# Performance work log

Hardware: AMD Instinct MI355X
Metric: run time of the kernel (lower is better)

Reference implementation:

```python
import jax, jax.numpy as jnp
import numpy as np

B, S, D, H, L, V, DFF = 8, 1024, 256, 8, 4, 100, 1024
EPS = 1e-5


def _pos_encodings(seq_len, d):
    # Faithful to SinusoidalPositionalEmbedding (NOTE: original uses sin for both halves)
    pos = jnp.arange(seq_len, dtype=jnp.float32)[:, None]        # [S,1]
    freqs = jnp.arange(d, dtype=jnp.float32)[None, :]            # [1,D]
    sin_even = jnp.sin(pos / 10000.0 ** (freqs[:, 0::2] / d))    # [S,D/2]
    sin_odd = jnp.sin(pos / 10000.0 ** (freqs[:, 1::2] / d))     # [S,D/2]
    return jnp.concatenate([sin_even, sin_odd], axis=1)          # [S,D]


def _self_attention_mask(sequence_length, seq_len):
    # create_self_attention_mask with causal=True; assumes max(sequence_length)==seq_len
    r = jnp.arange(seq_len)[None, :]                             # [1,S]
    m = (r < sequence_length[:, None]).astype(jnp.float32)       # [B,S]
    m = m[:, :, None] * m[:, None, :]                            # [B,S,S]
    causal = jnp.tril(jnp.ones((seq_len, seq_len), jnp.float32))
    return m * causal                                            # [B,S,S]


def setup_inputs() -> dict:
    key = jax.random.key(0)
    ks = jax.random.split(key, 20)
    n = lambda k, shape, s=0.02: (jax.random.normal(k, shape) * s).astype(jnp.float32)
    return {
        "output_ids": jax.random.randint(ks[0], (B, S), 0, V),
        "target_sequence_length": jnp.full((B,), S, dtype=jnp.int32),
        "embedding": n(ks[1], (V, D), 1.0),
        "Wq": n(ks[2], (L, D, D)), "bq": jnp.zeros((L, D), jnp.float32),
        "Wk": n(ks[3], (L, D, D)), "bk": jnp.zeros((L, D), jnp.float32),
        "Wv": n(ks[4], (L, D, D)), "bv": jnp.zeros((L, D), jnp.float32),
        "Wo": n(ks[5], (L, D, D)), "bo": jnp.zeros((L, D), jnp.float32),
        "W1": n(ks[6], (L, D, DFF)), "b1": jnp.zeros((L, DFF), jnp.float32),
        "W2": n(ks[7], (L, DFF, D)), "b2": jnp.zeros((L, D), jnp.float32),
        "g1": jnp.ones((L, D), jnp.float32), "be1": jnp.zeros((L, D), jnp.float32),
        "g2": jnp.ones((L, D), jnp.float32), "be2": jnp.zeros((L, D), jnp.float32),
        "Wc": n(ks[8], (D, V)), "bc": jnp.zeros((V,), jnp.float32),
    }


def _forward(output_ids, target_sequence_length, embedding, Wq, bq, Wk, bk, Wv, bv,
             Wo, bo, W1, b1, W2, b2, g1, be1, g2, be2, Wc, bc):
    Bn, Sn = output_ids.shape
    d = embedding.shape[1]
    x = embedding[output_ids] + _pos_encodings(Sn, d)[None]      # [B,S,D]
    mask = _self_attention_mask(target_sequence_length, Sn)[:, None] > 0  # [B,1,S,S] bool

    def ln(h, g, b):
        m = h.mean(-1, keepdims=True)
        v = jnp.var(h, axis=-1, keepdims=True)
        return (h - m) / jnp.sqrt(v + EPS) * g + b

    def step(x, p):
        wq, bq_, wk, bk_, wv, bv_, wo, bo_, w1, b1_, w2, b2_, g1_, be1_, g2_, be2_ = p
        q = (x @ wq + bq_).reshape(Bn, Sn, H, -1)
        k = (x @ wk + bk_).reshape(Bn, Sn, H, -1)
        v = (x @ wv + bv_).reshape(Bn, Sn, H, -1)
        dh = q.shape[-1]
        scores = jnp.einsum('bqhd,bkhd->bhqk', q, k) / jnp.sqrt(jnp.float32(dh))
        attn = jax.nn.softmax(jnp.where(mask, scores, -1e9), axis=-1)
        attn = jnp.where(mask, attn, 0.0)                        # post-softmax mask (as original)
        y = jnp.einsum('bhqk,bkhd->bqhd', attn, v).reshape(Bn, Sn, -1)
        y = y @ wo + bo_
        x = ln(x + y, g1_, be1_)
        ff = jax.nn.relu(x @ w1 + b1_) @ w2 + b2_
        x = ln(x + ff, g2_, be2_)
        return x, None

    x, _ = jax.lax.scan(step, x, (Wq, bq, Wk, bk, Wv, bv, Wo, bo, W1, b1, W2, b2, g1, be1, g2, be2))
    return x @ Wc + bc                                           # logits [B,S,V]


def reference(output_ids, target_sequence_length, embedding, Wq, bq, Wk, bk, Wv, bv,
              Wo, bo, W1, b1, W2, b2, g1, be1, g2, be2, Wc, bc):
    return _forward(output_ids, target_sequence_length, embedding, Wq, bq, Wk, bk, Wv, bv,
                    Wo, bo, W1, b1, W2, b2, g1, be1, g2, be2, Wc, bc)
```

## Files before the change

kernel.cpp:

```cpp
#include <hip/hip_runtime.h>
#include <hip/hip_bf16.h>
#include <stdint.h>

#define B_   8
#define S_   1024
#define D_   256
#define H_   8
#define DH_  32
#define L_   4
#define V_   100
#define DFF_ 1024
#define M_   (B_*S_)

using bf16 = __hip_bfloat16;
typedef __bf16 bf16x8 __attribute__((ext_vector_type(8)));
typedef float  f32x4  __attribute__((ext_vector_type(4)));

static __device__ __forceinline__ float b2f(unsigned short u) {
  union { unsigned int i; float f; } w; w.i = ((unsigned int)u) << 16; return w.f;
}

static __device__ __forceinline__ void load_lds16(const void* g, void* l) {
  __builtin_amdgcn_global_load_lds((const __attribute__((address_space(1))) void*)g,
                                   (__attribute__((address_space(3))) void*)l,
                                   16, 0, 0);
}

#define SRC_CHS(tid)  ((((tid) & 3) ^ (((tid) >> 3) & 3)) * 8)
#define FRAG_Q8(quad, l15)  (((quad) ^ (((l15) >> 1) & 3)) * 8)

template<int CTRL>
static __device__ __forceinline__ float dppf(float v) {
  union { float f; int i; } a, r;
  a.f = v;
  r.i = __builtin_amdgcn_update_dpp(0, a.i, CTRL, 0xF, 0xF, true);
  return r.f;
}
static __device__ __forceinline__ float red_sum16(float v) {
  v += dppf<0xB1>(v);
  v += dppf<0x4E>(v);
  v += dppf<0x141>(v);
  v += dppf<0x140>(v);
  return v;
}

__global__ void prep_t(const float* __restrict__ Wq, const float* __restrict__ Wk,
                       const float* __restrict__ Wv, const float* __restrict__ Wo,
                       const float* __restrict__ W1, const float* __restrict__ W2,
                       const float* __restrict__ Wc,
                       const float* __restrict__ bq, const float* __restrict__ bk,
                       const float* __restrict__ bv,
                       bf16* __restrict__ WqkvT, bf16* __restrict__ WoT,
                       bf16* __restrict__ W1T, bf16* __restrict__ W2T,
                       bf16* __restrict__ WcT, float* __restrict__ bqkv)
{
  const int z = blockIdx.z;
  if (z == 25) {
    if (blockIdx.x || blockIdx.y) return;
    const int tid = threadIdx.y*32 + threadIdx.x;
    for (int i = tid; i < L_*768; i += 256) {
      const int l2 = i / 768, j = i % 768;
      const float* src = (j < 256) ? bq : (j < 512) ? bk : bv;
      bqkv[i] = src[l2*256 + (j & 255)];
    }
    return;
  }
  const float* src; bf16* dst; int R, C, Cd;
  if (z < 12) {
    const int l = z / 3, w = z % 3;
    src = ((w == 0) ? Wq : (w == 1) ? Wk : Wv) + (size_t)l*65536;
    R = 256; C = 256; Cd = 256;
    dst = WqkvT + (size_t)l*196608 + (size_t)w*65536;
  } else if (z < 16) {
    const int l = z - 12;
    src = Wo + (size_t)l*65536; R = 256; C = 256; Cd = 256;
    dst = WoT + (size_t)l*65536;
  } else if (z < 20) {
    const int l = z - 16;
    src = W1 + (size_t)l*262144; R = 256; C = 1024; Cd = 1024;
    dst = W1T + (size_t)l*262144;
  } else if (z < 24) {
    const int l = z - 20;
    src = W2 + (size_t)l*262144; R = 1024; C = 256; Cd = 256;
    dst = W2T + (size_t)l*262144;
  } else {
    src = Wc; R = 256; C = 100; Cd = 128;
    dst = WcT;
  }
  const int c0 = blockIdx.x*32, r0 = blockIdx.y*32;
  if (c0 >= Cd || r0 >= R) return;
  __shared__ float t[32][33];
  #pragma unroll
  for (int i = 0; i < 4; ++i) {
    const int r = r0 + threadIdx.y + i*8;
    const int c = c0 + threadIdx.x;
    t[threadIdx.y + i*8][threadIdx.x] = (r < R && c < C) ? src[(size_t)r*C + c] : 0.f;
  }
  __syncthreads();
  #pragma unroll
  for (int i = 0; i < 4; ++i) {
    const int c = c0 + threadIdx.y + i*8;
    const int r = r0 + threadIdx.x;
    if (c < Cd && r < R)
      dst[(size_t)c*R + r] = (bf16)t[threadIdx.x][threadIdx.y + i*8];
  }
}

__global__ void embed_kernel(const int* __restrict__ ids, const float* __restrict__ emb,
                             bf16* __restrict__ x)
{
  const int bs = blockIdx.x;
  const int d  = threadIdx.x;
  const int s  = bs & (S_-1);
  const int id = ids[bs];
  const int f  = (d < 128) ? (2*d) : (2*(d-128)+1);
  const float inv = powf(10000.f, -(float)f * (1.f/256.f));
  const float pe  = sinf((float)s * inv);
  x[(size_t)bs*D_ + d] = (bf16)(emb[(size_t)id*D_ + d] + pe);
}

__global__ __launch_bounds__(256) void gemm_qkv(
    const bf16* __restrict__ A, const bf16* __restrict__ BT,
    const float* __restrict__ bias,
    bf16* __restrict__ qp, bf16* __restrict__ kp, bf16* __restrict__ vt)
{
  __shared__ bf16 As[128*32];
  __shared__ bf16 Bs[64*32];
  __shared__ bf16 Vs[64][136];
  const int tid  = threadIdx.x;
  const int lane = tid & 63, wave = tid >> 6;
  const int quad = lane >> 4, l15 = lane & 15;
  const int m0 = blockIdx.x * 128;
  const int n0 = blockIdx.y * 64;
  const int wm = (wave & 1) * 64;
  const int wn = (wave >> 1) * 32;
  const int K = 256;

  const bf16* a0 = A  + (size_t)m0 * K;
  const bf16* b0 = BT + (size_t)n0 * K;
  const int row = tid >> 2;
  const int chs = SRC_CHS(tid);
  const int q8  = FRAG_Q8(quad, l15);

  f32x4 acc[4][2] = {};

  for (int k0 = 0; k0 < K; k0 += 32) {
    __syncthreads();
    load_lds16(a0 + (size_t)row*K      + k0 + chs, (char*)As + (size_t)wave*1024);
    load_lds16(a0 + (size_t)(row+64)*K + k0 + chs, (char*)As + 4096 + (size_t)wave*1024);
    load_lds16(b0 + (size_t)row*K      + k0 + chs, (char*)Bs + (size_t)wave*1024);
    __syncthreads();
    bf16x8 af[4], bfr[2];
    #pragma unroll
    for (int mt = 0; mt < 4; ++mt)
      af[mt] = *(const bf16x8*)(As + (wm + mt*16 + l15)*32 + q8);
    #pragma unroll
    for (int nt = 0; nt < 2; ++nt)
      bfr[nt] = *(const bf16x8*)(Bs + (wn + nt*16 + l15)*32 + q8);
    #pragma unroll
    for (int mt = 0; mt < 4; ++mt)
      #pragma unroll
      for (int nt = 0; nt < 2; ++nt)
        acc[mt][nt] = __builtin_amdgcn_mfma_f32_16x16x32_bf16(af[mt], bfr[nt], acc[mt][nt], 0, 0, 0);
  }

  const int seg = n0 >> 8;
  const int b  = m0 >> 10;
  const int s0 = m0 & 1023;

  if (seg < 2) {
    bf16* dst = seg ? kp : qp;
    const float sc = seg ? 1.f : 0.17677669529663687f;
    #pragma unroll
    for (int nt = 0; nt < 2; ++nt) {
      const int n  = n0 + wn + nt*16 + l15;
      const int nn = n & 255;
      const int h = nn >> 5, d = nn & 31;
      const float bvs = bias[n];
      bf16* hb = dst + (((size_t)b*H_ + h)*S_)*DH_ + d;
      #pragma unroll
      for (int mt = 0; mt < 4; ++mt) {
        const int ml = wm + mt*16 + quad*4;
        #pragma unroll
        for (int r = 0; r < 4; ++r)
          hb[(size_t)(s0 + ml + r)*DH_] = (bf16)((acc[mt][nt][r] + bvs) * sc);
      }
    }
  } else {
    #pragma unroll
    for (int nt = 0; nt < 2; ++nt) {
      const int nl = wn + nt*16 + l15;
      const float bvs = bias[n0 + nl];
      #pragma unroll
      for (int mt = 0; mt < 4; ++mt) {
        const int ml = wm + mt*16 + quad*4;
        #pragma unroll
        for (int r = 0; r < 4; ++r)
          Vs[nl][ml + r] = (bf16)(acc[mt][nt][r] + bvs);
      }
    }
    __syncthreads();
    #pragma unroll
    for (int t = 0; t < 2; ++t) {
      const int vrow = (tid >> 3) + 32*t;
      const int soff = (tid & 7) * 16;
      const int nn = (n0 + vrow) & 255;
      const int h = nn >> 5, d = nn & 31;
      bf16* dst = vt + (((size_t)b*H_ + h)*DH_ + d)*S_ + s0 + soff;
      *(bf16x8*)dst       = *(const bf16x8*)&Vs[vrow][soff];
      *(bf16x8*)(dst + 8) = *(const bf16x8*)&Vs[vrow][soff + 8];
    }
  }
}

template<bool RELU, bool OUT_BF16>
__global__ __launch_bounds__(256) void gemm_bt(
    const bf16* __restrict__ A, const bf16* __restrict__ BT,
    const float* __restrict__ bias, void* __restrict__ C,
    int M, int N, int K)
{
  __shared__ bf16 As[128*32];
  __shared__ bf16 Bs[64*32];
  const int tid  = threadIdx.x;
  const int lane = tid & 63, wave = tid >> 6;
  const int quad = lane >> 4, l15 = lane & 15;
  const int m0 = blockIdx.x * 128;
  const int n0 = blockIdx.y * 64;
  const int wm = (wave & 1) * 64;
  const int wn = (wave >> 1) * 32;

  const bf16* a0 = A  + (size_t)m0 * K;
  const bf16* b0 = BT + (size_t)n0 * K;
  const int row = tid >> 2;
  const int chs = SRC_CHS(tid);
  const int q8  = FRAG_Q8(quad, l15);

  f32x4 acc[4][2] = {};

  for (int k0 = 0; k0 < K; k0 += 32) {
    __syncthreads();
    load_lds16(a0 + (size_t)row*K      + k0 + chs, (char*)As + (size_t)wave*1024);
    load_lds16(a0 + (size_t)(row+64)*K + k0 + chs, (char*)As + 4096 + (size_t)wave*1024);
    load_lds16(b0 + (size_t)row*K      + k0 + chs, (char*)Bs + (size_t)wave*1024);
    __syncthreads();
    bf16x8 af[4], bfr[2];
    #pragma unroll
    for (int mt = 0; mt < 4; ++mt)
      af[mt] = *(const bf16x8*)(As + (wm + mt*16 + l15)*32 + q8);
    #pragma unroll
    for (int nt = 0; nt < 2; ++nt)
      bfr[nt] = *(const bf16x8*)(Bs + (wn + nt*16 + l15)*32 + q8);
    #pragma unroll
    for (int mt = 0; mt < 4; ++mt)
      #pragma unroll
      for (int nt = 0; nt < 2; ++nt)
        acc[mt][nt] = __builtin_amdgcn_mfma_f32_16x16x32_bf16(af[mt], bfr[nt], acc[mt][nt], 0, 0, 0);
  }

  #pragma unroll
  for (int nt = 0; nt < 2; ++nt) {
    const int n = n0 + wn + nt*16 + l15;
    const float bvs = bias[n];
    #pragma unroll
    for (int mt = 0; mt < 4; ++mt) {
      const int mr = m0 + wm + mt*16 + quad*4;
      #pragma unroll
      for (int r = 0; r < 4; ++r) {
        float v = acc[mt][nt][r] + bvs;
        if (RELU) v = fmaxf(v, 0.f);
        if (OUT_BF16) ((bf16*)C)[(size_t)(mr + r)*N + n] = (bf16)v;
        else          ((float*)C)[(size_t)(mr + r)*N + n] = v;
      }
    }
  }
}

template<bool RELU, bool OUT_BF16, bool NMASK>
__global__ __launch_bounds__(256) void gemm_bt64(
    const bf16* __restrict__ A, const bf16* __restrict__ BT,
    const float* __restrict__ bias, void* __restrict__ C,
    int M, int N, int K)
{
  __shared__ bf16 As[64*32];
  __shared__ bf16 Bs[64*32];
  const int tid  = threadIdx.x;
  const int lane = tid & 63, wave = tid >> 6;
  const int quad = lane >> 4, l15 = lane & 15;
  const int m0 = blockIdx.x * 64;
  const int n0 = blockIdx.y * 64;
  const int wm = (wave & 1) * 32;
  const int wn = (wave >> 1) * 32;

  const bf16* a0 = A  + (size_t)m0 * K;
  const bf16* b0 = BT + (size_t)n0 * K;
  const int row = tid >> 2;
  const int chs = SRC_CHS(tid);
  const int q8  = FRAG_Q8(quad, l15);

  f32x4 acc[2][2] = {};

  for (int k0 = 0; k0 < K; k0 += 32) {
    __syncthreads();
    load_lds16(a0 + (size_t)row*K + k0 + chs, (char*)As + (size_t)wave*1024);
    load_lds16(b0 + (size_t)row*K + k0 + chs, (char*)Bs + (size_t)wave*1024);
    __syncthreads();
    bf16x8 af[2], bfr[2];
    #pragma unroll
    for (int mt = 0; mt < 2; ++mt)
      af[mt] = *(const bf16x8*)(As + (wm + mt*16 + l15)*32 + q8);
    #pragma unroll
    for (int nt = 0; nt < 2; ++nt)
      bfr[nt] = *(const bf16x8*)(Bs + (wn + nt*16 + l15)*32 + q8);
    #pragma unroll
    for (int mt = 0; mt < 2; ++mt)
      #pragma unroll
      for (int nt = 0; nt < 2; ++nt)
        acc[mt][nt] = __builtin_amdgcn_mfma_f32_16x16x32_bf16(af[mt], bfr[nt], acc[mt][nt], 0, 0, 0);
  }

  #pragma unroll
  for (int nt = 0; nt < 2; ++nt) {
    const int n = n0 + wn + nt*16 + l15;
    if (NMASK && n >= N) continue;
    const float bvs = bias[n];
    #pragma unroll
    for (int mt = 0; mt < 2; ++mt) {
      const int mr = m0 + wm + mt*16 + quad*4;
      #pragma unroll
      for (int r = 0; r < 4; ++r) {
        float v = acc[mt][nt][r] + bvs;
        if (RELU) v = fmaxf(v, 0.f);
        if (OUT_BF16) ((bf16*)C)[(size_t)(mr + r)*N + n] = (bf16)v;
        else          ((float*)C)[(size_t)(mr + r)*N + n] = v;
      }
    }
  }
}

__global__ __launch_bounds__(256) void gemm_ln(
    const bf16* __restrict__ A, const bf16* __restrict__ BT,
    const float* __restrict__ bias, const float* __restrict__ g,
    const float* __restrict__ be, bf16* xio, int K)
{
  __shared__ bf16 As[16*32];
  __shared__ bf16 Bs[256*32];
  __shared__ bf16 Xs[16][264];
  __shared__ float sums[4][16][2];

  const int tid  = threadIdx.x;
  const int lane = tid & 63, wave = tid >> 6;
  const int quad = lane >> 4, l15 = lane & 15;
  const int m0 = blockIdx.x * 16;
  const int wn = wave * 64;

  const bf16* a0 = A + (size_t)m0 * K;
  const int chs = SRC_CHS(tid);
  const int q8  = FRAG_Q8(quad, l15);

  f32x4 acc[4] = {};

  for (int k0 = 0; k0 < K; k0 += 32) {
    __syncthreads();
    if (wave == 0)
      load_lds16(a0 + (size_t)(lane >> 2)*K + k0 + SRC_CHS(lane), (char*)As);
    #pragma unroll
    for (int j = 0; j < 4; ++j)
      load_lds16(BT + (size_t)(64*j + (tid >> 2))*K + k0 + chs,
                 (char*)Bs + j*4096 + (size_t)wave*1024);
    __syncthreads();
    const bf16x8 af = *(const bf16x8*)(As + l15*32 + q8);
    #pragma unroll
    for (int nt = 0; nt < 4; ++nt) {
      const bf16x8 bfr = *(const bf16x8*)(Bs + (wn + nt*16 + l15)*32 + q8);
      acc[nt] = __builtin_amdgcn_mfma_f32_16x16x32_bf16(af, bfr, acc[nt], 0, 0, 0);
    }
  }

  {
    const int xr = tid >> 4, xc = (tid & 15) * 16;
    const bf16* src = xio + (size_t)(m0 + xr)*D_ + xc;
    *(bf16x8*)&Xs[xr][xc]     = *(const bf16x8*)src;
    *(bf16x8*)&Xs[xr][xc + 8] = *(const bf16x8*)(src + 8);
  }
  __syncthreads();

  float v[4][4];
  float bvs[4];
  #pragma unroll
  for (int nt = 0; nt < 4; ++nt) bvs[nt] = bias[wn + nt*16 + l15];
  #pragma unroll
  for (int r = 0; r < 4; ++r) {
    const int rr = quad*4 + r;
    float ls = 0.f, lq = 0.f;
    #pragma unroll
    for (int nt = 0; nt < 4; ++nt) {
      const float y = acc[nt][r] + bvs[nt];
      const float xv = b2f(*(const unsigned short*)&Xs[rr][wn + nt*16 + l15]);
      const float vv = xv + y;
      v[r][nt] = vv;
      ls += vv;
      lq += vv*vv;
    }
    ls = red_sum16(ls);
    lq = red_sum16(lq);
    if (l15 == 0) { sums[wave][rr][0] = ls; sums[wave][rr][1] = lq; }
  }
  __syncthreads();

  float gv[4], bev[4];
  #pragma unroll
  for (int nt = 0; nt < 4; ++nt) {
    gv[nt]  = g[wn + nt*16 + l15];
    bev[nt] = be[wn + nt*16 + l15];
  }
  #pragma unroll
  for (int r = 0; r < 4; ++r) {
    const int rr = quad*4 + r;
    const float ts = sums[0][rr][0] + sums[1][rr][0] + sums[2][rr][0] + sums[3][rr][0];
    const float tq = sums[0][rr][1] + sums[1][rr][1] + sums[2][rr][1] + sums[3][rr][1];
    const float mean = ts * (1.f/256.f);
    const float var  = tq * (1.f/256.f) - mean*mean;
    const float inv  = rsqrtf(var + 1e-5f);
    #pragma unroll
    for (int nt = 0; nt < 4; ++nt) {
      const bf16 o = (bf16)((v[r][nt] - mean)*inv*gv[nt] + bev[nt]);
      Xs[rr][wn + nt*16 + l15] = o;
    }
  }
  __syncthreads();

  {
    const int xr = tid >> 4, xc = (tid & 15) * 16;
    bf16* dst = xio + (size_t)(m0 + xr)*D_ + xc;
    *(bf16x8*)dst       = *(const bf16x8*)&Xs[xr][xc];
    *(bf16x8*)(dst + 8) = *(const bf16x8*)&Xs[xr][xc + 8];
  }
}

#define PSTR 68
__global__ __launch_bounds__(256) void attn_kernel(
    const bf16* __restrict__ qp, const bf16* __restrict__ kp,
    const bf16* __restrict__ vt, const int* __restrict__ tsl,
    bf16* __restrict__ out)
{
  const int h = blockIdx.y, b = blockIdx.z;
  const int lane = threadIdx.x & 63, wave = threadIdx.x >> 6;
  const int quad = lane >> 4, l15 = lane & 15;
  const int sid = blockIdx.x + wave*16;
  const int q0 = sid*16;
  const int len = tsl[b];

  __shared__ bf16 Pl[4][16*PSTR];

  const size_t bh = (size_t)b*H_ + h;
  const bf16* qb = qp + bh*S_*DH_;
  const bf16* kb = kp + bh*S_*DH_;
  const bf16* vb = vt + bh*DH_*S_;

  const bf16x8 qf = *(const bf16x8*)(qb + (size_t)(q0 + l15)*DH_ + quad*8);

  float lacc[4] = {0.f, 0.f, 0.f, 0.f};
  f32x4 o0 = {0.f,0.f,0.f,0.f}, o1 = {0.f,0.f,0.f,0.f};

  bf16* pw = &Pl[wave][0];
  const int qrow0 = q0 + quad*4;
  const bool full = (len >= S_);
  const int dt = sid >> 2;

  for (int ks = 0; ks <= dt; ++ks) {
    const int k0 = ks*64;
    f32x4 s[4];
    #pragma unroll
    for (int nt = 0; nt < 4; ++nt) {
      const bf16x8 kf = *(const bf16x8*)(kb + (size_t)(k0 + nt*16 + l15)*DH_ + quad*8);
      const f32x4 z = {0.f,0.f,0.f,0.f};
      s[nt] = __builtin_amdgcn_mfma_f32_16x16x32_bf16(qf, kf, z, 0, 0, 0);
    }
    float p[4][4];
    if (full && ks < dt) {
      #pragma unroll
      for (int nt = 0; nt < 4; ++nt)
        #pragma unroll
        for (int r = 0; r < 4; ++r)
          p[nt][r] = __expf(s[nt][r]);
    } else {
      #pragma unroll
      for (int nt = 0; nt < 4; ++nt) {
        const int kpos = k0 + nt*16 + l15;
        #pragma unroll
        for (int r = 0; r < 4; ++r) {
          const int qr = qrow0 + r;
          const bool ok = (kpos <= qr) && (kpos < len) && (qr < len);
          p[nt][r] = ok ? __expf(s[nt][r]) : 0.f;
        }
      }
    }
    #pragma unroll
    for (int r = 0; r < 4; ++r)
      lacc[r] += (p[0][r] + p[1][r]) + (p[2][r] + p[3][r]);
    #pragma unroll
    for (int nt = 0; nt < 4; ++nt)
      #pragma unroll
      for (int r = 0; r < 4; ++r)
        pw[(quad*4+r)*PSTR + nt*16 + l15] = (bf16)p[nt][r];
    asm volatile("s_waitcnt lgkmcnt(0)" ::: "memory");
    #pragma unroll
    for (int kc = 0; kc < 2; ++kc) {
      const bf16x8 pf = *(const bf16x8*)(pw + l15*PSTR + kc*32 + quad*8);
      const bf16x8 vf0 = *(const bf16x8*)(vb + (size_t)l15*S_ + k0 + kc*32 + quad*8);
      o0 = __builtin_amdgcn_mfma_f32_16x16x32_bf16(pf, vf0, o0, 0, 0, 0);
      const bf16x8 vf1 = *(const bf16x8*)(vb + (size_t)(16 + l15)*S_ + k0 + kc*32 + quad*8);
      o1 = __builtin_amdgcn_mfma_f32_16x16x32_bf16(pf, vf1, o1, 0, 0, 0);
    }
  }

  bf16* ob = out + (size_t)b*S_*D_ + h*DH_;
  #pragma unroll
  for (int r = 0; r < 4; ++r) {
    const float l = red_sum16(lacc[r]);
    const float inv = 1.f / fmaxf(l, 1e-30f);
    const size_t rowoff = (size_t)(q0 + quad*4 + r)*D_;
    ob[rowoff + l15]      = (bf16)(o0[r]*inv);
    ob[rowoff + 16 + l15] = (bf16)(o1[r]*inv);
  }
}

extern "C" void kernel_launch(void* const* d_in, const int* in_sizes, int n_in,
                              void* d_out, int out_size, void* d_ws, size_t ws_size,
                              hipStream_t stream)
{
  const int*   ids = (const int*)d_in[0];
  const int*   tsl = (const int*)d_in[1];
  const float* emb = (const float*)d_in[2];
  const float* Wq  = (const float*)d_in[3];
  const float* bq  = (const float*)d_in[4];
  const float* Wk  = (const float*)d_in[5];
  const float* bk  = (const float*)d_in[6];
  const float* Wv  = (const float*)d_in[7];
  const float* bv  = (const float*)d_in[8];
  const float* Wo  = (const float*)d_in[9];
  const float* bo  = (const float*)d_in[10];
  const float* W1  = (const float*)d_in[11];
  const float* b1  = (const float*)d_in[12];
  const float* W2  = (const float*)d_in[13];
  const float* b2  = (const float*)d_in[14];
  const float* g1  = (const float*)d_in[15];
  const float* be1 = (const float*)d_in[16];
  const float* g2  = (const float*)d_in[17];
  const float* be2 = (const float*)d_in[18];
  const float* Wc  = (const float*)d_in[19];
  const float* bc  = (const float*)d_in[20];

  if (ws_size < (size_t)40*1024*1024) return;

  char* p = (char*)d_ws;
  auto carve = [&](size_t bytes) { void* r = (void*)p; p += (bytes + 255) & ~(size_t)255; return r; };
  bf16*  x     = (bf16*) carve((size_t)M_*D_*2);
  char*  big   = (char*) carve((size_t)M_*DFF_*2);
  char*  pkbuf = (char*) carve((size_t)12*1024*1024);
  bf16*  WqkvT = (bf16*) carve((size_t)L_*768*256*2);
  bf16*  WoT   = (bf16*) carve((size_t)L_*65536*2);
  bf16*  W1T   = (bf16*) carve((size_t)L_*262144*2);
  bf16*  W2T   = (bf16*) carve((size_t)L_*262144*2);
  bf16*  WcT   = (bf16*) carve((size_t)128*256*2);
  float* bqkv  = (float*)carve((size_t)L_*768*4);

  bf16*  aout = (bf16*)big;
  bf16*  ff1  = (bf16*)big;
  bf16*  qp   = (bf16*)pkbuf;
  bf16*  kp   = (bf16*)(pkbuf + (size_t)4*1024*1024);
  bf16*  vt   = (bf16*)(pkbuf + (size_t)8*1024*1024);

  prep_t<<<dim3(32,32,26), dim3(32,8), 0, stream>>>(Wq,Wk,Wv,Wo,W1,W2,Wc,bq,bk,bv,
                                                    WqkvT,WoT,W1T,W2T,WcT,bqkv);
  embed_kernel<<<dim3(M_), 256, 0, stream>>>(ids, emb, x);

  for (int l = 0; l < L_; ++l) {
    gemm_qkv<<<dim3(64,12), 256, 0, stream>>>(
        x, WqkvT + (size_t)l*768*256, bqkv + l*768, qp, kp, vt);
    attn_kernel<<<dim3(16,8,8), 256, 0, stream>>>(qp, kp, vt, tsl, aout);
    gemm_ln<<<dim3(512), 256, 0, stream>>>(
        aout, WoT + (size_t)l*65536, bo + l*256, g1 + l*256, be1 + l*256, x, 256);
    gemm_bt<true,true><<<dim3(64,16), 256, 0, stream>>>(
        x, W1T + (size_t)l*262144, b1 + l*1024, ff1, M_, 1024, 256);
    gemm_ln<<<dim3(512), 256, 0, stream>>>(
        ff1, W2T + (size_t)l*262144, b2 + l*256, g2 + l*256, be2 + l*256, x, 1024);
  }

  gemm_bt64<false,false,true><<<dim3(128,2), 256, 0, stream>>>(
      x, WcT, bc, (float*)d_out, M_, V_, 256);
}
```

Baseline: 464.6 us.

## Transpose QK^T MFMA, use exp2 with folded log2e, prefetch K/V tiles

The Q projection scale now folds in log2(e), so the attention kernel can use exp2f in place of __expf. The score MFMA operands are swapped so each lane holds one query row with four consecutive keys. This lets P be packed into 8-byte LDS stores and the row sum be reduced with two cross-lane shuffles. K fragments for the next tile and V fragments for the current tile are loaded before they are needed, overlapping global load latency with the MFMA and exp work, at the cost of more registers.

```diff
diff --git a/kernel.cpp b/kernel.cpp
--- a/kernel.cpp
+++ b/kernel.cpp
@@ -18,6 +18,9 @@
 
 static __device__ __forceinline__ float b2f(unsigned short u) {
   union { unsigned int i; float f; } w; w.i = ((unsigned int)u) << 16; return w.f;
+}
+static __device__ __forceinline__ unsigned short f2b(float f) {
+  bf16 h = (bf16)f; return *(unsigned short*)&h;
 }
 
 static __device__ __forceinline__ void load_lds16(const void* g, void* l) {
@@ -170,7 +173,7 @@
 
   if (seg < 2) {
     bf16* dst = seg ? kp : qp;
-    const float sc = seg ? 1.f : 0.17677669529663687f;
+    const float sc = seg ? 1.f : (0.17677669529663687f * 1.4426950408889634f);
     #pragma unroll
     for (int nt = 0; nt < 2; ++nt) {
       const int n  = n0 + wn + nt*16 + l15;
@@ -459,66 +462,84 @@
 
   const bf16x8 qf = *(const bf16x8*)(qb + (size_t)(q0 + l15)*DH_ + quad*8);
 
-  float lacc[4] = {0.f, 0.f, 0.f, 0.f};
+  float lacc = 0.f;
   f32x4 o0 = {0.f,0.f,0.f,0.f}, o1 = {0.f,0.f,0.f,0.f};
 
   bf16* pw = &Pl[wave][0];
-  const int qrow0 = q0 + quad*4;
+  const int qr = q0 + l15;
   const bool full = (len >= S_);
   const int dt = sid >> 2;
 
+  bf16x8 kf[4];
+  #pragma unroll
+  for (int nt = 0; nt < 4; ++nt)
+    kf[nt] = *(const bf16x8*)(kb + (size_t)(nt*16 + l15)*DH_ + quad*8);
+
   for (int ks = 0; ks <= dt; ++ks) {
     const int k0 = ks*64;
+    bf16x8 vf[4];
+    #pragma unroll
+    for (int kc = 0; kc < 2; ++kc) {
+      vf[kc*2]   = *(const bf16x8*)(vb + (size_t)l15*S_      + k0 + kc*32 + quad*8);
+      vf[kc*2+1] = *(const bf16x8*)(vb + (size_t)(16+l15)*S_ + k0 + kc*32 + quad*8);
+    }
     f32x4 s[4];
     #pragma unroll
     for (int nt = 0; nt < 4; ++nt) {
-      const bf16x8 kf = *(const bf16x8*)(kb + (size_t)(k0 + nt*16 + l15)*DH_ + quad*8);
       const f32x4 z = {0.f,0.f,0.f,0.f};
-      s[nt] = __builtin_amdgcn_mfma_f32_16x16x32_bf16(qf, kf, z, 0, 0, 0);
-    }
-    float p[4][4];
-    if (full && ks < dt) {
+      s[nt] = __builtin_amdgcn_mfma_f32_16x16x32_bf16(kf[nt], qf, z, 0, 0, 0);
+    }
+    bf16x8 kn[4];
+    if (ks < dt) {
+      const int k1 = k0 + 64;
       #pragma unroll
       for (int nt = 0; nt < 4; ++nt)
-        #pragma unroll
-        for (int r = 0; r < 4; ++r)
-          p[nt][r] = __expf(s[nt][r]);
-    } else {
-      #pragma unroll
-      for (int nt = 0; nt < 4; ++nt) {
-        const int kpos = k0 + nt*16 + l15;
-        #pragma unroll
-        for (int r = 0; r < 4; ++r) {
-          const int qr = qrow0 + r;
-          const bool ok = (kpos <= qr) && (kpos < len) && (qr < len);
-          p[nt][r] = ok ? __expf(s[nt][r]) : 0.f;
-        }
+        kn[nt] = *(const bf16x8*)(kb + (size_t)(k1 + nt*16 + l15)*DH_ + quad*8);
+    }
+    #pragma unroll
+    for (int nt = 0; nt < 4; ++nt) {
+      float p0, p1, p2, p3;
+      if (full && ks < dt) {
+        p0 = exp2f(s[nt][0]);
+        p1 = exp2f(s[nt][1]);
+        p2 = exp2f(s[nt][2]);
+        p3 = exp2f(s[nt][3]);
+      } else {
+        const int kbase = k0 + nt*16 + quad*4;
+        const bool okq = (qr < len);
+        p0 = (okq && kbase+0 <= qr && kbase+0 < len) ? exp2f(s[nt][0]) : 0.f;
+        p1 = (okq && kbase+1 <= qr && kbase+1 < len) ? exp2f(s[nt][1]) : 0.f;
+        p2 = (okq && kbase+2 <= qr && kbase+2 < len) ? exp2f(s[nt][2]) : 0.f;
+        p3 = (okq && kbase+3 <= qr && kbase+3 < len) ? exp2f(s[nt][3]) : 0.f;
       }
-    }
-    #pragma unroll
-    for (int r = 0; r < 4; ++r)
-      lacc[r] += (p[0][r] + p[1][r]) + (p[2][r] + p[3][r]);
-    #pragma unroll
-    for (int nt = 0; nt < 4; ++nt)
-      #pragma unroll
-      for (int r = 0; r < 4; ++r)
-        pw[(quad*4+r)*PSTR + nt*16 + l15] = (bf16)p[nt][r];
+      lacc += (p0 + p1) + (p2 + p3);
+      uint2 w;
+      w.x = (unsigned)f2b(p0) | ((unsigned)f2b(p1) << 16);
+      w.y = (unsigned)f2b(p2) | ((unsigned)f2b(p3) << 16);
+      *(uint2*)((char*)pw + l15*(PSTR*2) + nt*32 + quad*8) = w;
+    }
     asm volatile("s_waitcnt lgkmcnt(0)" ::: "memory");
     #pragma unroll
     for (int kc = 0; kc < 2; ++kc) {
       const bf16x8 pf = *(const bf16x8*)(pw + l15*PSTR + kc*32 + quad*8);
-      const bf16x8 vf0 = *(const bf16x8*)(vb + (size_t)l15*S_ + k0 + kc*32 + quad*8);
-      o0 = __builtin_amdgcn_mfma_f32_16x16x32_bf16(pf, vf0, o0, 0, 0, 0);
-      const bf16x8 vf1 = *(const bf16x8*)(vb + (size_t)(16 + l15)*S_ + k0 + kc*32 + quad*8);
-      o1 = __builtin_amdgcn_mfma_f32_16x16x32_bf16(pf, vf1, o1, 0, 0, 0);
-    }
-  }
+      o0 = __builtin_amdgcn_mfma_f32_16x16x32_bf16(pf, vf[kc*2],   o0, 0, 0, 0);
+      o1 = __builtin_amdgcn_mfma_f32_16x16x32_bf16(pf, vf[kc*2+1], o1, 0, 0, 0);
+    }
+    if (ks < dt) {
+      #pragma unroll
+      for (int nt = 0; nt < 4; ++nt) kf[nt] = kn[nt];
+    }
+  }
+
+  float lt = lacc;
+  lt += __shfl_xor(lt, 16);
+  lt += __shfl_xor(lt, 32);
 
   bf16* ob = out + (size_t)b*S_*D_ + h*DH_;
   #pragma unroll
   for (int r = 0; r < 4; ++r) {
-    const float l = red_sum16(lacc[r]);
-    const float inv = 1.f / fmaxf(l, 1e-30f);
+    const float lr = __shfl(lt, (lane & 48) | (quad*4 + r));
+    const float inv = 1.f / fmaxf(lr, 1e-30f);
     const size_t rowoff = (size_t)(q0 + quad*4 + r)*D_;
     ob[rowoff + l15]      = (bf16)(o0[r]*inv);
     ob[rowoff + 16 + l15] = (bf16)(o1[r]*inv);
```

After: 464.1 us. Within noise of the previous version (-0.1%).
